# Kernel tuning notes

Measured on AMD Instinct MI355X. Metric: run time of the kernel, lower is better.

## Reference

```python
import jax, jax.numpy as jnp
import numpy as np

NPOINT = 2048
NSAMPLE = 32
BN_EPS = 1e-5


def fps(xyz_t, npoint):
    """Furthest point sampling. xyz_t: [B,N,3] -> idx [B,npoint] (starts at index 0)."""
    B, N, _ = xyz_t.shape

    def step(carry, _):
        dist, last = carry  # dist [B,N], last [B]
        centroid = jnp.take_along_axis(xyz_t, last[:, None, None], axis=1)  # [B,1,3]
        d = jnp.sum((xyz_t - centroid) ** 2, axis=-1)  # [B,N]
        dist = jnp.minimum(dist, d)
        nxt = jnp.argmax(dist, axis=1).astype(jnp.int32)
        return (dist, nxt), last

    init = (jnp.full((B, N), 1e10, xyz_t.dtype), jnp.zeros((B,), jnp.int32))
    _, idx = jax.lax.scan(step, init, None, length=npoint)  # [npoint,B]
    return jnp.transpose(idx)  # [B,npoint]


def knn(k, query_t, ref_t):
    """query_t [B,S,3], ref_t [B,N,3] -> k-nearest indices [B,S,k]."""
    d = (jnp.sum(query_t ** 2, -1)[:, :, None]
         + jnp.sum(ref_t ** 2, -1)[:, None, :]
         - 2.0 * jnp.einsum('bsc,bnc->bsn', query_t, ref_t))  # [B,S,N]
    _, idx = jax.lax.top_k(-d, k)
    return idx


def group(feat_t, idx):
    """feat_t [B,N,C], idx [B,S,K] -> [B,S,K,C] gathered neighbors."""
    return jax.vmap(lambda f, i: f[i])(feat_t, idx)


def setup_inputs():
    key = jax.random.key(0)
    ks = jax.random.split(key, 8)
    B, N, C, D = 8, 8192, 3, 3
    mlp = [32, 32, 64]
    inp = {
        'xyz': jax.random.normal(ks[0], (B, C, N), jnp.float32),
        'points': jax.random.normal(ks[1], (B, D, N), jnp.float32),
    }
    last = D + 3  # conv input channels = in_channel + 3
    for i, oc in enumerate(mlp):
        inp[f'w{i}'] = jax.random.normal(ks[2 + i], (oc, last), jnp.float32) * (1.0 / np.sqrt(last))
        inp[f'g{i}'] = jnp.ones((oc,), jnp.float32)
        inp[f'b{i}'] = jnp.zeros((oc,), jnp.float32)
        last = oc
    return inp


def reference(xyz, points, w0, g0, b0, w1, g1, b1, w2, g2, b2):
    xyz_t = jnp.transpose(xyz, (0, 2, 1))        # [B,N,3]
    points_t = jnp.transpose(points, (0, 2, 1))  # [B,N,D]

    fps_idx = fps(xyz_t, NPOINT)                             # [B,S]
    new_xyz_t = jax.vmap(lambda f, i: f[i])(xyz_t, fps_idx)  # [B,S,3]

    knn_idx = knn(NSAMPLE, new_xyz_t, xyz_t)                 # [B,S,K]
    grouped_xyz = group(xyz_t, knn_idx)                      # [B,S,K,3]
    pos_diff = grouped_xyz - new_xyz_t[:, :, None, :]        # [B,S,K,3]
    grouped_pts = group(points_t, knn_idx)                   # [B,S,K,D]

    x = jnp.concatenate([pos_diff, grouped_pts], axis=-1)    # [B,S,K,3+D]
    for w, g, b in ((w0, g0, b0), (w1, g1, b1), (w2, g2, b2)):
        x = jnp.einsum('oc,bskc->bsko', w, x)                # 1x1 conv, no bias
        mean = jnp.mean(x, axis=(0, 1, 2))                   # BatchNorm2d (training stats)
        var = jnp.var(x, axis=(0, 1, 2))
        x = jax.nn.relu(g * (x - mean) * jax.lax.rsqrt(var + BN_EPS) + b)

    new_points = jnp.max(x, axis=2)  # max over K neighbors -> [B,S,C']
    new_xyz = jnp.transpose(new_xyz_t, (0, 2, 1))      # [B,3,S]
    new_points = jnp.transpose(new_points, (0, 2, 1))  # [B,C',S]
    return (new_xyz, new_points, fps_idx)
```

## Files before the change

kernel.cpp:

```cpp
#include <hip/hip_runtime.h>
#include <hip/hip_bf16.h>
#include <math.h>


#define NB 8
#define NN 8192
#define NS 2048
#define NK 32

__global__ __launch_bounds__(256) void prep_kernel(const float* __restrict__ xyz,
                                                   const float* __restrict__ pts,
                                                   float4* __restrict__ xyz4,
                                                   float4* __restrict__ pts4) {
  int g = blockIdx.x * 256 + threadIdx.x;
  int b = g >> 13, n = g & 8191;
  const float* xb = xyz + b * 3 * NN;
  float x = xb[n], y = xb[NN + n], z = xb[2 * NN + n];
  xyz4[g] = make_float4(x, y, z, fmaf(x, x, fmaf(y, y, z * z)));
  const float* pb = pts + b * 3 * NN;
  pts4[g] = make_float4(pb[n], pb[NN + n], pb[2 * NN + n], 0.f);
}

template <int CTRL>
__device__ __forceinline__ float dpp_max(float v) {
  int o = __builtin_amdgcn_update_dpp(__float_as_int(v), __float_as_int(v),
                                      CTRL, 0xf, 0xf, false);
  return fmaxf(v, __int_as_float(o));
}

__global__ __launch_bounds__(512, 2) void fps_kernel(const float4* __restrict__ xyz4,
                                                     float* __restrict__ out_nxyz,
                                                     float* __restrict__ out_fps,
                                                     float4* __restrict__ nxyz4) {
  __shared__ unsigned long long wslot[2][8];
  int b = blockIdx.x, tid = threadIdx.x;
  int lane = tid & 63, wid = tid >> 6;
  const float4* xb = xyz4 + b * NN;

  float ax[16], ay[16], az[16];
  float dist[16];
#pragma unroll
  for (int j = 0; j < 16; ++j) {
    float4 t = xb[(tid << 4) + j];
    asm volatile("v_accvgpr_write_b32 %0, %1" : "=a"(ax[j]) : "v"(t.x));
    asm volatile("v_accvgpr_write_b32 %0, %1" : "=a"(ay[j]) : "v"(t.y));
    asm volatile("v_accvgpr_write_b32 %0, %1" : "=a"(az[j]) : "v"(t.z));
    dist[j] = 1e10f;
  }

  float4 c0 = xb[0];
  float cx = c0.x, cy = c0.y, cz = c0.z;
  if (tid == 0) {
    nxyz4[b * NS] = c0;
    out_nxyz[b * 3 * NS] = c0.x;
    out_nxyz[b * 3 * NS + NS] = c0.y;
    out_nxyz[b * 3 * NS + 2 * NS] = c0.z;
    out_fps[b * NS] = 0.f;
  }
  __syncthreads();

  for (int s = 1; s < NS; ++s) {
    float best = -1.0f;
    int bj = 0;
#pragma unroll
    for (int j = 0; j < 16; ++j) {
      float x, y, z;
      asm volatile("v_accvgpr_read_b32 %0, %1" : "=v"(x) : "a"(ax[j]));
      asm volatile("v_accvgpr_read_b32 %0, %1" : "=v"(y) : "a"(ay[j]));
      asm volatile("v_accvgpr_read_b32 %0, %1" : "=v"(z) : "a"(az[j]));
      float dx = __fsub_rn(x, cx);
      float dy = __fsub_rn(y, cy);
      float dz = __fsub_rn(z, cz);
      float d = __fadd_rn(__fadd_rn(__fmul_rn(dx, dx), __fmul_rn(dy, dy)),
                          __fmul_rn(dz, dz));
      d = fminf(dist[j], d);
      dist[j] = d;
      bool gt = d > best;
      best = gt ? d : best;
      bj = gt ? j : bj;
    }

    float m = best;
    m = dpp_max<0x111>(m);
    m = dpp_max<0x112>(m);
    m = dpp_max<0x114>(m);
    m = dpp_max<0x118>(m);
    m = dpp_max<0x142>(m);
    m = dpp_max<0x143>(m);
    float wmax = __int_as_float(__builtin_amdgcn_readlane(__float_as_int(m), 63));

    unsigned long long bl = __ballot(best == wmax);
    int l0 = __ffsll(bl) - 1;
    int gcand = (tid << 4) + bj;
    int gw = __builtin_amdgcn_readlane(gcand, l0);

    if (lane == 0)
      wslot[s & 1][wid] = (((unsigned long long)__float_as_uint(wmax)) << 32) |
                          (unsigned)(8191 - gw);
    __syncthreads();

    unsigned long long vm = wslot[s & 1][0];
#pragma unroll
    for (int k = 1; k < 8; ++k) {
      unsigned long long o = wslot[s & 1][k];
      vm = o > vm ? o : vm;
    }
    int gid = 8191 - (int)(unsigned)(vm & 0xFFFFFFFFull);
    gid = __builtin_amdgcn_readfirstlane(gid);

    float4 c = xb[gid];
    cx = c.x; cy = c.y; cz = c.z;
    if (tid == 0) {
      nxyz4[b * NS + s] = c;
      out_nxyz[b * 3 * NS + s] = c.x;
      out_nxyz[b * 3 * NS + NS + s] = c.y;
      out_nxyz[b * 3 * NS + 2 * NS + s] = c.z;
      out_fps[b * NS + s] = (float)gid;
    }
  }
}

__device__ __forceinline__ void insert32(float (&a)[32], float f) {
#pragma unroll
  for (int i = 31; i >= 1; --i) a[i] = fminf(a[i], fmaxf(a[i - 1], f));
  a[0] = fminf(a[0], f);
}

__global__ __launch_bounds__(256) void knn_kernel(const float4* __restrict__ xyz4,
                                                  const float4* __restrict__ nxyz4,
                                                  int* __restrict__ knn) {
  __shared__ float lbuf[256][33];
  int b = blockIdx.x >> 5, tile = blockIdx.x & 31;
  int tid = threadIdx.x;
  int q = tid & 63, chunk = tid >> 6;
  float4 Q = nxyz4[b * NS + tile * 64 + q];
  float qq = Q.w;
  float mx = -2.f * Q.x, my = -2.f * Q.y, mz = -2.f * Q.z;
  float arr[32];
#pragma unroll
  for (int i = 0; i < 32; ++i) arr[i] = __uint_as_float(0x7f7fffffu);

  const float4* refs = xyz4 + b * NN + chunk * 2048;
  int rbase = chunk * 2048;
  for (int r = 0; r < 2048; r += 4) {
    float4 R0 = refs[r];
    float4 R1 = refs[r + 1];
    float4 R2 = refs[r + 2];
    float4 R3 = refs[r + 3];
    float d0 = fmaxf(fmaf(R0.x, mx, fmaf(R0.y, my, fmaf(R0.z, mz, R0.w + qq))), 0.f);
    float d1 = fmaxf(fmaf(R1.x, mx, fmaf(R1.y, my, fmaf(R1.z, mz, R1.w + qq))), 0.f);
    float d2 = fmaxf(fmaf(R2.x, mx, fmaf(R2.y, my, fmaf(R2.z, mz, R2.w + qq))), 0.f);
    float d3 = fmaxf(fmaf(R3.x, mx, fmaf(R3.y, my, fmaf(R3.z, mz, R3.w + qq))), 0.f);
    float f0 = __uint_as_float((__float_as_uint(d0) & 0xFFFFE000u) | (unsigned)(rbase + r));
    float f1 = __uint_as_float((__float_as_uint(d1) & 0xFFFFE000u) | (unsigned)(rbase + r + 1));
    float f2 = __uint_as_float((__float_as_uint(d2) & 0xFFFFE000u) | (unsigned)(rbase + r + 2));
    float f3 = __uint_as_float((__float_as_uint(d3) & 0xFFFFE000u) | (unsigned)(rbase + r + 3));
    if (f0 < arr[31]) insert32(arr, f0);
    if (f1 < arr[31]) insert32(arr, f1);
    if (f2 < arr[31]) insert32(arr, f2);
    if (f3 < arr[31]) insert32(arr, f3);
  }
#pragma unroll
  for (int i = 0; i < 32; ++i) lbuf[tid][i] = arr[i];
  __syncthreads();
  if (tid < 64) {
    for (int c = 1; c < 4; ++c)
      for (int i = 0; i < 32; ++i) {
        float f = lbuf[c * 64 + tid][i];
        if (f < arr[31]) insert32(arr, f);
      }
    int base = (b * NS + tile * 64 + tid) * NK;
#pragma unroll
    for (int i = 0; i < 32; ++i) knn[base + i] = (int)(__float_as_uint(arr[i]) & 0x1FFFu);
  }
}

template <int STAGE>
__global__ __launch_bounds__(256) void mlp_kernel(
    const float4* __restrict__ xyz4, const float4* __restrict__ pts4,
    const float4* __restrict__ nxyz4, const int* __restrict__ knn,
    const float* __restrict__ w0, const float* __restrict__ w1,
    const float* __restrict__ w2, const float* __restrict__ ab,
    float* __restrict__ partials, float* __restrict__ out_np) {
  constexpr int C = (STAGE == 2) ? 64 : 32;
  constexpr int SM = (STAGE == 3) ? 8 * 64 * 32 : 512;
  __shared__ float smem[SM];
  int blk = blockIdx.x;
  int b = blk >> 6, s0 = (blk & 63) * 32;
  int tid = threadIdx.x, sl = tid & 31, ksec = tid >> 5;
  int lane = tid & 63, wid = tid >> 6;
  int s = s0 + sl;
  float4 Q = nxyz4[b * NS + s];
  const float4* xb = xyz4 + b * NN;
  const float4* pb = pts4 + b * NN;
  const int* kb = knn + (b * NS + s) * NK + ksec * 4;

  float acc1[(STAGE == 3) ? 64 : C];
  float acc2[(STAGE == 3) ? 1 : C];
  if constexpr (STAGE == 3) {
#pragma unroll
    for (int o = 0; o < 64; ++o) acc1[o] = -3.4e38f;
  } else {
#pragma unroll
    for (int o = 0; o < C; ++o) { acc1[o] = 0.f; acc2[o] = 0.f; }
  }

  for (int kk = 0; kk < 4; ++kk) {
    int nid = kb[kk];
    float4 R = xb[nid];
    float4 P = pb[nid];
    float x0[6] = {R.x - Q.x, R.y - Q.y, R.z - Q.z, P.x, P.y, P.z};
    float h[32];
#pragma unroll
    for (int o = 0; o < 32; ++o) {
      float a = w0[o * 6] * x0[0];
#pragma unroll
      for (int c = 1; c < 6; ++c) a = fmaf(w0[o * 6 + c], x0[c], a);
      h[o] = a;
    }
    if constexpr (STAGE == 0) {
#pragma unroll
      for (int o = 0; o < 32; ++o) { acc1[o] += h[o]; acc2[o] = fmaf(h[o], h[o], acc2[o]); }
    } else {
#pragma unroll
      for (int o = 0; o < 32; ++o) h[o] = fmaxf(fmaf(h[o], ab[o], ab[64 + o]), 0.f);
      float h1[32];
#pragma unroll
      for (int o = 0; o < 32; ++o) {
        float a = 0.f;
#pragma unroll
        for (int i = 0; i < 32; ++i) a = fmaf(w1[o * 32 + i], h[i], a);
        h1[o] = a;
      }
      if constexpr (STAGE == 1) {
#pragma unroll
        for (int o = 0; o < 32; ++o) { acc1[o] += h1[o]; acc2[o] = fmaf(h1[o], h1[o], acc2[o]); }
      } else {
#pragma unroll
        for (int o = 0; o < 32; ++o) h1[o] = fmaxf(fmaf(h1[o], ab[128 + o], ab[192 + o]), 0.f);
#pragma unroll
        for (int o = 0; o < 64; ++o) {
          float a = 0.f;
#pragma unroll
          for (int i = 0; i < 32; ++i) a = fmaf(w2[o * 32 + i], h1[i], a);
          if constexpr (STAGE == 2) {
            acc1[o] += a;
            acc2[o] = fmaf(a, a, acc2[o]);
          } else {
            acc1[o] = fmaxf(acc1[o], fmaxf(fmaf(a, ab[256 + o], ab[320 + o]), 0.f));
          }
        }
      }
    }
  }

  if constexpr (STAGE < 3) {
#pragma unroll
    for (int o = 0; o < C; ++o) {
      float v1 = acc1[o], v2 = acc2[o];
#pragma unroll
      for (int d = 1; d < 64; d <<= 1) { v1 += __shfl_xor(v1, d); v2 += __shfl_xor(v2, d); }
      acc1[o] = v1; acc2[o] = v2;
    }
    if (lane == 0) {
#pragma unroll
      for (int o = 0; o < C; ++o) {
        smem[wid * 2 * C + o] = acc1[o];
        smem[wid * 2 * C + C + o] = acc2[o];
      }
    }
    __syncthreads();
    if (tid < 2 * C) {
      float v = smem[tid] + smem[2 * C + tid] + smem[4 * C + tid] + smem[6 * C + tid];
      partials[blk * 128 + tid] = v;
    }
  } else {
#pragma unroll
    for (int o = 0; o < 64; ++o) smem[ksec * 2048 + o * 32 + sl] = acc1[o];
    __syncthreads();
#pragma unroll
    for (int i = 0; i < 8; ++i) {
      int e = i * 256 + tid;
      int ch = e >> 5, ss = e & 31;
      float v = smem[ch * 32 + ss];
#pragma unroll
      for (int ks = 1; ks < 8; ++ks) v = fmaxf(v, smem[ks * 2048 + ch * 32 + ss]);
      out_np[b * 64 * NS + ch * NS + s0 + ss] = v;
    }
  }
}

__global__ __launch_bounds__(256) void finalize_kernel(const float* __restrict__ partials,
                                                       const float* __restrict__ g,
                                                       const float* __restrict__ bt,
                                                       float* __restrict__ ab, int C) {
  __shared__ float sm[256];
  int tid = threadIdx.x;
  int ch = tid & 127, half = tid >> 7;
  float acc = 0.f;
  if (ch < 2 * C) {
    const float* p = partials + half * 256 * 128 + ch;
    for (int i = 0; i < 256; ++i) acc += p[i * 128];
  }
  sm[half * 128 + ch] = acc;
  __syncthreads();
  if (tid < C) {
    float s1 = sm[tid] + sm[128 + tid];
    float s2 = sm[C + tid] + sm[128 + C + tid];
    const float ninv = 1.0f / 524288.0f;
    float mean = s1 * ninv;
    float var = s2 * ninv - mean * mean;
    float inv = 1.0f / sqrtf(var + 1e-5f);
    float a = g[tid] * inv;
    ab[tid] = a;
    ab[64 + tid] = bt[tid] - mean * a;
  }
}

extern "C" void kernel_launch(void* const* d_in, const int* in_sizes, int n_in,
                              void* d_out, int out_size, void* d_ws, size_t ws_size,
                              hipStream_t stream) {
  const float* xyz = (const float*)d_in[0];
  const float* pts = (const float*)d_in[1];
  const float* w0 = (const float*)d_in[2];
  const float* g0 = (const float*)d_in[3];
  const float* b0 = (const float*)d_in[4];
  const float* w1 = (const float*)d_in[5];
  const float* g1 = (const float*)d_in[6];
  const float* b1 = (const float*)d_in[7];
  const float* w2 = (const float*)d_in[8];
  const float* g2 = (const float*)d_in[9];
  const float* b2 = (const float*)d_in[10];
  float* out = (float*)d_out;
  float* ws = (float*)d_ws;

  float4* xyz4 = (float4*)ws;
  float4* pts4 = (float4*)(ws + 262144);
  float4* nxyz4 = (float4*)(ws + 524288);
  int* knn = (int*)(ws + 589824);
  float* partials = ws + 1114112;
  float* ab = ws + 1310720;
  float* out_np = out + 49152;
  float* out_fps = out + 1097728;

  prep_kernel<<<256, 256, 0, stream>>>(xyz, pts, xyz4, pts4);
  fps_kernel<<<NB, 512, 0, stream>>>(xyz4, out, out_fps, nxyz4);
  knn_kernel<<<256, 256, 0, stream>>>(xyz4, nxyz4, knn);

  mlp_kernel<0><<<512, 256, 0, stream>>>(xyz4, pts4, nxyz4, knn, w0, w1, w2, ab, partials, nullptr);
  finalize_kernel<<<1, 256, 0, stream>>>(partials, g0, b0, ab, 32);
  mlp_kernel<1><<<512, 256, 0, stream>>>(xyz4, pts4, nxyz4, knn, w0, w1, w2, ab, partials + 65536, nullptr);
  finalize_kernel<<<1, 256, 0, stream>>>(partials + 65536, g1, b1, ab + 128, 32);
  mlp_kernel<2><<<512, 256, 0, stream>>>(xyz4, pts4, nxyz4, knn, w0, w1, w2, ab, partials + 131072, nullptr);
  finalize_kernel<<<1, 256, 0, stream>>>(partials + 131072, g2, b2, ab + 256, 64);
  mlp_kernel<3><<<512, 256, 0, stream>>>(xyz4, pts4, nxyz4, knn, w0, w1, w2, ab, nullptr, out_np);
}
```

Baseline: 3.265 ms.

## Fuse FPS, KNN and first BN stats into one persistent kernel with progress flags

Merges the FPS, KNN and stage-0 MLP statistics into a single mega-kernel. Eight blocks run FPS and publish progress every 64 samples through a release flag, while the KNN blocks spin-wait on that flag and start as soon as their tile of centroids exists. This overlaps KNN with the serial FPS loop and removes the separate mlp stage-0 pass. The per-block partial buffers are replaced by global atomicAdd accumulation, which shrinks the finalize kernel, and the FPS argmax is restructured to a max pass plus a search on the winning lane only. The spin-wait needs every FPS block to be resident alongside the waiting blocks; if the 8 FPS blocks are not scheduled, the kernel deadlocks.

```diff
diff --git a/kernel.cpp b/kernel.cpp
--- a/kernel.cpp
+++ b/kernel.cpp
@@ -11,8 +11,15 @@
 __global__ __launch_bounds__(256) void prep_kernel(const float* __restrict__ xyz,
                                                    const float* __restrict__ pts,
                                                    float4* __restrict__ xyz4,
-                                                   float4* __restrict__ pts4) {
-  int g = blockIdx.x * 256 + threadIdx.x;
+                                                   float4* __restrict__ pts4,
+                                                   float* __restrict__ stats_acc,
+                                                   int* __restrict__ prog) {
+  int tid = threadIdx.x;
+  if (blockIdx.x == 0) {
+    stats_acc[tid] = 0.f;
+    if (tid < 8) prog[tid] = 0;
+  }
+  int g = blockIdx.x * 256 + tid;
   int b = g >> 13, n = g & 8191;
   const float* xb = xyz + b * 3 * NN;
   float x = xb[n], y = xb[NN + n], z = xb[2 * NN + n];
@@ -28,140 +35,158 @@
   return fmaxf(v, __int_as_float(o));
 }
 
-__global__ __launch_bounds__(512, 2) void fps_kernel(const float4* __restrict__ xyz4,
-                                                     float* __restrict__ out_nxyz,
-                                                     float* __restrict__ out_fps,
-                                                     float4* __restrict__ nxyz4) {
-  __shared__ unsigned long long wslot[2][8];
-  int b = blockIdx.x, tid = threadIdx.x;
-  int lane = tid & 63, wid = tid >> 6;
-  const float4* xb = xyz4 + b * NN;
-
-  float ax[16], ay[16], az[16];
-  float dist[16];
-#pragma unroll
-  for (int j = 0; j < 16; ++j) {
-    float4 t = xb[(tid << 4) + j];
-    asm volatile("v_accvgpr_write_b32 %0, %1" : "=a"(ax[j]) : "v"(t.x));
-    asm volatile("v_accvgpr_write_b32 %0, %1" : "=a"(ay[j]) : "v"(t.y));
-    asm volatile("v_accvgpr_write_b32 %0, %1" : "=a"(az[j]) : "v"(t.z));
-    dist[j] = 1e10f;
-  }
-
-  float4 c0 = xb[0];
-  float cx = c0.x, cy = c0.y, cz = c0.z;
-  if (tid == 0) {
-    nxyz4[b * NS] = c0;
-    out_nxyz[b * 3 * NS] = c0.x;
-    out_nxyz[b * 3 * NS + NS] = c0.y;
-    out_nxyz[b * 3 * NS + 2 * NS] = c0.z;
-    out_fps[b * NS] = 0.f;
-  }
-  __syncthreads();
-
-  for (int s = 1; s < NS; ++s) {
-    float best = -1.0f;
-    int bj = 0;
-#pragma unroll
-    for (int j = 0; j < 16; ++j) {
-      float x, y, z;
-      asm volatile("v_accvgpr_read_b32 %0, %1" : "=v"(x) : "a"(ax[j]));
-      asm volatile("v_accvgpr_read_b32 %0, %1" : "=v"(y) : "a"(ay[j]));
-      asm volatile("v_accvgpr_read_b32 %0, %1" : "=v"(z) : "a"(az[j]));
-      float dx = __fsub_rn(x, cx);
-      float dy = __fsub_rn(y, cy);
-      float dz = __fsub_rn(z, cz);
-      float d = __fadd_rn(__fadd_rn(__fmul_rn(dx, dx), __fmul_rn(dy, dy)),
-                          __fmul_rn(dz, dz));
-      d = fminf(dist[j], d);
-      dist[j] = d;
-      bool gt = d > best;
-      best = gt ? d : best;
-      bj = gt ? j : bj;
-    }
-
-    float m = best;
-    m = dpp_max<0x111>(m);
-    m = dpp_max<0x112>(m);
-    m = dpp_max<0x114>(m);
-    m = dpp_max<0x118>(m);
-    m = dpp_max<0x142>(m);
-    m = dpp_max<0x143>(m);
-    float wmax = __int_as_float(__builtin_amdgcn_readlane(__float_as_int(m), 63));
-
-    unsigned long long bl = __ballot(best == wmax);
-    int l0 = __ffsll(bl) - 1;
-    int gcand = (tid << 4) + bj;
-    int gw = __builtin_amdgcn_readlane(gcand, l0);
-
-    if (lane == 0)
-      wslot[s & 1][wid] = (((unsigned long long)__float_as_uint(wmax)) << 32) |
-                          (unsigned)(8191 - gw);
-    __syncthreads();
-
-    unsigned long long vm = wslot[s & 1][0];
-#pragma unroll
-    for (int k = 1; k < 8; ++k) {
-      unsigned long long o = wslot[s & 1][k];
-      vm = o > vm ? o : vm;
-    }
-    int gid = 8191 - (int)(unsigned)(vm & 0xFFFFFFFFull);
-    gid = __builtin_amdgcn_readfirstlane(gid);
-
-    float4 c = xb[gid];
-    cx = c.x; cy = c.y; cz = c.z;
-    if (tid == 0) {
-      nxyz4[b * NS + s] = c;
-      out_nxyz[b * 3 * NS + s] = c.x;
-      out_nxyz[b * 3 * NS + NS + s] = c.y;
-      out_nxyz[b * 3 * NS + 2 * NS + s] = c.z;
-      out_fps[b * NS + s] = (float)gid;
-    }
-  }
-}
-
 __device__ __forceinline__ void insert32(float (&a)[32], float f) {
 #pragma unroll
   for (int i = 31; i >= 1; --i) a[i] = fminf(a[i], fmaxf(a[i - 1], f));
   a[0] = fminf(a[0], f);
 }
 
-__global__ __launch_bounds__(256) void knn_kernel(const float4* __restrict__ xyz4,
-                                                  const float4* __restrict__ nxyz4,
-                                                  int* __restrict__ knn) {
+__global__ __launch_bounds__(512, 1) void mega_kernel(
+    const float4* __restrict__ xyz4, const float4* __restrict__ pts4,
+    float4* __restrict__ nxyz4, int* __restrict__ knn,
+    const float* __restrict__ w0, float* __restrict__ stats_acc,
+    int* __restrict__ prog, float* __restrict__ out_nxyz,
+    float* __restrict__ out_fps) {
   __shared__ float lbuf[256][33];
-  int b = blockIdx.x >> 5, tile = blockIdx.x & 31;
+  __shared__ unsigned long long wslot[2][8];
   int tid = threadIdx.x;
-  int q = tid & 63, chunk = tid >> 6;
-  float4 Q = nxyz4[b * NS + tile * 64 + q];
-  float qq = Q.w;
-  float mx = -2.f * Q.x, my = -2.f * Q.y, mz = -2.f * Q.z;
+  int lane = tid & 63, wid = tid >> 6;
+
+  if (blockIdx.x < 8) {
+    int b = blockIdx.x;
+    const float4* xb = xyz4 + b * NN;
+
+    float ax[16], ay[16], az[16], dist[16];
+#pragma unroll
+    for (int j = 0; j < 16; ++j) {
+      float4 t = xb[(tid << 4) + j];
+      asm volatile("v_accvgpr_write_b32 %0, %1" : "=a"(ax[j]) : "v"(t.x));
+      asm volatile("v_accvgpr_write_b32 %0, %1" : "=a"(ay[j]) : "v"(t.y));
+      asm volatile("v_accvgpr_write_b32 %0, %1" : "=a"(az[j]) : "v"(t.z));
+      dist[j] = 1e10f;
+    }
+    float4 c0 = xb[0];
+    float cx = c0.x, cy = c0.y, cz = c0.z;
+    if (tid == 0) {
+      nxyz4[b * NS] = c0;
+      out_nxyz[b * 3 * NS] = c0.x;
+      out_nxyz[b * 3 * NS + NS] = c0.y;
+      out_nxyz[b * 3 * NS + 2 * NS] = c0.z;
+      out_fps[b * NS] = 0.f;
+    }
+    __syncthreads();
+
+    for (int s = 1; s < NS; ++s) {
+#pragma unroll
+      for (int j = 0; j < 16; ++j) {
+        float x, y, z;
+        asm volatile("v_accvgpr_read_b32 %0, %1" : "=v"(x) : "a"(ax[j]));
+        asm volatile("v_accvgpr_read_b32 %0, %1" : "=v"(y) : "a"(ay[j]));
+        asm volatile("v_accvgpr_read_b32 %0, %1" : "=v"(z) : "a"(az[j]));
+        float dx = __fsub_rn(x, cx);
+        float dy = __fsub_rn(y, cy);
+        float dz = __fsub_rn(z, cz);
+        float d = __fadd_rn(__fadd_rn(__fmul_rn(dx, dx), __fmul_rn(dy, dy)),
+                            __fmul_rn(dz, dz));
+        dist[j] = fminf(dist[j], d);
+      }
+      float lmax = dist[0];
+#pragma unroll
+      for (int j = 1; j < 16; ++j) lmax = fmaxf(lmax, dist[j]);
+
+      float m = lmax;
+      m = dpp_max<0x111>(m);
+      m = dpp_max<0x112>(m);
+      m = dpp_max<0x114>(m);
+      m = dpp_max<0x118>(m);
+      m = dpp_max<0x142>(m);
+      m = dpp_max<0x143>(m);
+      float wmax = __int_as_float(__builtin_amdgcn_readlane(__float_as_int(m), 63));
+
+      unsigned long long bl = __ballot(lmax == wmax);
+      int l0 = __ffsll(bl) - 1;
+      int bj = 0;
+      if (lmax == wmax) {
+#pragma unroll
+        for (int t = 15; t >= 0; --t)
+          if (dist[t] == lmax) bj = t;
+      }
+      int gcand = (tid << 4) + bj;
+      int gw = __builtin_amdgcn_readlane(gcand, l0);
+
+      if (lane == 0)
+        wslot[s & 1][wid] = (((unsigned long long)__float_as_uint(wmax)) << 32) |
+                            (unsigned)(8191 - gw);
+      __syncthreads();
+
+      unsigned long long vm = wslot[s & 1][0];
+#pragma unroll
+      for (int k = 1; k < 8; ++k) {
+        unsigned long long o = wslot[s & 1][k];
+        vm = o > vm ? o : vm;
+      }
+      int gid = 8191 - (int)(unsigned)(vm & 0xFFFFFFFFull);
+      gid = __builtin_amdgcn_readfirstlane(gid);
+
+      float4 c = xb[gid];
+      cx = c.x; cy = c.y; cz = c.z;
+      if (tid == 0) {
+        nxyz4[b * NS + s] = c;
+        out_nxyz[b * 3 * NS + s] = c.x;
+        out_nxyz[b * 3 * NS + NS + s] = c.y;
+        out_nxyz[b * 3 * NS + 2 * NS + s] = c.z;
+        out_fps[b * NS + s] = (float)gid;
+        if (((s + 1) & 63) == 0) {
+          __threadfence();
+          __hip_atomic_store(&prog[b], s + 1, __ATOMIC_RELEASE,
+                             __HIP_MEMORY_SCOPE_AGENT);
+        }
+      }
+    }
+    return;
+  }
+
+  int idx = blockIdx.x - 8;
+  int b = idx >> 5, tile = idx & 31;
+  const float4* xb = xyz4 + b * NN;
+  const float4* pb = pts4 + b * NN;
+
+  if (tid == 0) {
+    int need = (tile + 1) * 64;
+    while (__hip_atomic_load(&prog[b], __ATOMIC_ACQUIRE,
+                             __HIP_MEMORY_SCOPE_AGENT) < need)
+      __builtin_amdgcn_s_sleep(64);
+  }
+  __syncthreads();
+
   float arr[32];
-#pragma unroll
-  for (int i = 0; i < 32; ++i) arr[i] = __uint_as_float(0x7f7fffffu);
-
-  const float4* refs = xyz4 + b * NN + chunk * 2048;
-  int rbase = chunk * 2048;
-  for (int r = 0; r < 2048; r += 4) {
-    float4 R0 = refs[r];
-    float4 R1 = refs[r + 1];
-    float4 R2 = refs[r + 2];
-    float4 R3 = refs[r + 3];
-    float d0 = fmaxf(fmaf(R0.x, mx, fmaf(R0.y, my, fmaf(R0.z, mz, R0.w + qq))), 0.f);
-    float d1 = fmaxf(fmaf(R1.x, mx, fmaf(R1.y, my, fmaf(R1.z, mz, R1.w + qq))), 0.f);
-    float d2 = fmaxf(fmaf(R2.x, mx, fmaf(R2.y, my, fmaf(R2.z, mz, R2.w + qq))), 0.f);
-    float d3 = fmaxf(fmaf(R3.x, mx, fmaf(R3.y, my, fmaf(R3.z, mz, R3.w + qq))), 0.f);
-    float f0 = __uint_as_float((__float_as_uint(d0) & 0xFFFFE000u) | (unsigned)(rbase + r));
-    float f1 = __uint_as_float((__float_as_uint(d1) & 0xFFFFE000u) | (unsigned)(rbase + r + 1));
-    float f2 = __uint_as_float((__float_as_uint(d2) & 0xFFFFE000u) | (unsigned)(rbase + r + 2));
-    float f3 = __uint_as_float((__float_as_uint(d3) & 0xFFFFE000u) | (unsigned)(rbase + r + 3));
-    if (f0 < arr[31]) insert32(arr, f0);
-    if (f1 < arr[31]) insert32(arr, f1);
-    if (f2 < arr[31]) insert32(arr, f2);
-    if (f3 < arr[31]) insert32(arr, f3);
-  }
-#pragma unroll
-  for (int i = 0; i < 32; ++i) lbuf[tid][i] = arr[i];
+  if (tid < 256) {
+    int q = tid & 63, chunk = tid >> 6;
+    float4 Q = nxyz4[b * NS + tile * 64 + q];
+    float qq = Q.w;
+    float mx = -2.f * Q.x, my = -2.f * Q.y, mz = -2.f * Q.z;
+#pragma unroll
+    for (int i = 0; i < 32; ++i) arr[i] = __uint_as_float(0x7f7fffffu);
+    const float4* refs = xb + chunk * 2048;
+    int rbase = chunk * 2048;
+    for (int r = 0; r < 2048; r += 4) {
+      float4 R0 = refs[r], R1 = refs[r + 1], R2 = refs[r + 2], R3 = refs[r + 3];
+      float d0 = fmaxf(fmaf(R0.x, mx, fmaf(R0.y, my, fmaf(R0.z, mz, R0.w + qq))), 0.f);
+      float d1 = fmaxf(fmaf(R1.x, mx, fmaf(R1.y, my, fmaf(R1.z, mz, R1.w + qq))), 0.f);
+      float d2 = fmaxf(fmaf(R2.x, mx, fmaf(R2.y, my, fmaf(R2.z, mz, R2.w + qq))), 0.f);
+      float d3 = fmaxf(fmaf(R3.x, mx, fmaf(R3.y, my, fmaf(R3.z, mz, R3.w + qq))), 0.f);
+      float f0 = __uint_as_float((__float_as_uint(d0) & 0xFFFFE000u) | (unsigned)(rbase + r));
+      float f1 = __uint_as_float((__float_as_uint(d1) & 0xFFFFE000u) | (unsigned)(rbase + r + 1));
+      float f2 = __uint_as_float((__float_as_uint(d2) & 0xFFFFE000u) | (unsigned)(rbase + r + 2));
+      float f3 = __uint_as_float((__float_as_uint(d3) & 0xFFFFE000u) | (unsigned)(rbase + r + 3));
+      if (f0 < arr[31]) insert32(arr, f0);
+      if (f1 < arr[31]) insert32(arr, f1);
+      if (f2 < arr[31]) insert32(arr, f2);
+      if (f3 < arr[31]) insert32(arr, f3);
+    }
+#pragma unroll
+    for (int i = 0; i < 32; ++i) lbuf[tid][i] = arr[i];
+  }
   __syncthreads();
   if (tid < 64) {
     for (int c = 1; c < 4; ++c)
@@ -171,7 +196,55 @@
       }
     int base = (b * NS + tile * 64 + tid) * NK;
 #pragma unroll
-    for (int i = 0; i < 32; ++i) knn[base + i] = (int)(__float_as_uint(arr[i]) & 0x1FFFu);
+    for (int i = 0; i < 32; ++i) {
+      knn[base + i] = (int)(__float_as_uint(arr[i]) & 0x1FFFu);
+      lbuf[tid][i] = arr[i];
+    }
+  }
+  __syncthreads();
+
+  float sum[32], sumsq[32];
+#pragma unroll
+  for (int o = 0; o < 32; ++o) { sum[o] = 0.f; sumsq[o] = 0.f; }
+  for (int t = 0; t < 4; ++t) {
+    int e = tid * 4 + t;
+    int sq = e >> 5, k = e & 31;
+    int nid = (int)(__float_as_uint(lbuf[sq][k]) & 0x1FFFu);
+    float4 Q = nxyz4[b * NS + tile * 64 + sq];
+    float4 R = xb[nid];
+    float4 P = pb[nid];
+    float x0[6] = {R.x - Q.x, R.y - Q.y, R.z - Q.z, P.x, P.y, P.z};
+#pragma unroll
+    for (int o = 0; o < 32; ++o) {
+      float a = w0[o * 6] * x0[0];
+#pragma unroll
+      for (int c = 1; c < 6; ++c) a = fmaf(w0[o * 6 + c], x0[c], a);
+      sum[o] += a;
+      sumsq[o] = fmaf(a, a, sumsq[o]);
+    }
+  }
+#pragma unroll
+  for (int o = 0; o < 32; ++o) {
+    float s = sum[o], q = sumsq[o];
+#pragma unroll
+    for (int d = 1; d < 64; d <<= 1) { s += __shfl_xor(s, d); q += __shfl_xor(q, d); }
+    sum[o] = s; sumsq[o] = q;
+  }
+  __syncthreads();
+  float* cmb = &lbuf[0][0];
+  if (lane == 0) {
+#pragma unroll
+    for (int o = 0; o < 32; ++o) {
+      cmb[wid * 64 + o] = sum[o];
+      cmb[wid * 64 + 32 + o] = sumsq[o];
+    }
+  }
+  __syncthreads();
+  if (tid < 64) {
+    float tot = 0.f;
+#pragma unroll
+    for (int w = 0; w < 8; ++w) tot += cmb[w * 64 + tid];
+    atomicAdd(&stats_acc[tid], tot);
   }
 }
 
@@ -181,7 +254,7 @@
     const float4* __restrict__ nxyz4, const int* __restrict__ knn,
     const float* __restrict__ w0, const float* __restrict__ w1,
     const float* __restrict__ w2, const float* __restrict__ ab,
-    float* __restrict__ partials, float* __restrict__ out_np) {
+    float* __restrict__ acc, float* __restrict__ out_np) {
   constexpr int C = (STAGE == 2) ? 64 : 32;
   constexpr int SM = (STAGE == 3) ? 8 * 64 * 32 : 512;
   __shared__ float smem[SM];
@@ -216,39 +289,32 @@
       float a = w0[o * 6] * x0[0];
 #pragma unroll
       for (int c = 1; c < 6; ++c) a = fmaf(w0[o * 6 + c], x0[c], a);
-      h[o] = a;
-    }
-    if constexpr (STAGE == 0) {
-#pragma unroll
-      for (int o = 0; o < 32; ++o) { acc1[o] += h[o]; acc2[o] = fmaf(h[o], h[o], acc2[o]); }
+      h[o] = fmaxf(fmaf(a, ab[o], ab[64 + o]), 0.f);
+    }
+    float h1[32];
+#pragma unroll
+    for (int o = 0; o < 32; ++o) {
+      float a = 0.f;
+#pragma unroll
+      for (int i = 0; i < 32; ++i) a = fmaf(w1[o * 32 + i], h[i], a);
+      h1[o] = a;
+    }
+    if constexpr (STAGE == 1) {
+#pragma unroll
+      for (int o = 0; o < 32; ++o) { acc1[o] += h1[o]; acc2[o] = fmaf(h1[o], h1[o], acc2[o]); }
     } else {
 #pragma unroll
-      for (int o = 0; o < 32; ++o) h[o] = fmaxf(fmaf(h[o], ab[o], ab[64 + o]), 0.f);
-      float h1[32];
-#pragma unroll
-      for (int o = 0; o < 32; ++o) {
+      for (int o = 0; o < 32; ++o) h1[o] = fmaxf(fmaf(h1[o], ab[128 + o], ab[192 + o]), 0.f);
+#pragma unroll
+      for (int o = 0; o < 64; ++o) {
         float a = 0.f;
 #pragma unroll
-        for (int i = 0; i < 32; ++i) a = fmaf(w1[o * 32 + i], h[i], a);
-        h1[o] = a;
-      }
-      if constexpr (STAGE == 1) {
-#pragma unroll
-        for (int o = 0; o < 32; ++o) { acc1[o] += h1[o]; acc2[o] = fmaf(h1[o], h1[o], acc2[o]); }
-      } else {
-#pragma unroll
-        for (int o = 0; o < 32; ++o) h1[o] = fmaxf(fmaf(h1[o], ab[128 + o], ab[192 + o]), 0.f);
-#pragma unroll
-        for (int o = 0; o < 64; ++o) {
-          float a = 0.f;
-#pragma unroll
-          for (int i = 0; i < 32; ++i) a = fmaf(w2[o * 32 + i], h1[i], a);
-          if constexpr (STAGE == 2) {
-            acc1[o] += a;
-            acc2[o] = fmaf(a, a, acc2[o]);
-          } else {
-            acc1[o] = fmaxf(acc1[o], fmaxf(fmaf(a, ab[256 + o], ab[320 + o]), 0.f));
-          }
+        for (int i = 0; i < 32; ++i) a = fmaf(w2[o * 32 + i], h1[i], a);
+        if constexpr (STAGE == 2) {
+          acc1[o] += a;
+          acc2[o] = fmaf(a, a, acc2[o]);
+        } else {
+          acc1[o] = fmaxf(acc1[o], fmaxf(fmaf(a, ab[256 + o], ab[320 + o]), 0.f));
         }
       }
     }
@@ -272,7 +338,7 @@
     __syncthreads();
     if (tid < 2 * C) {
       float v = smem[tid] + smem[2 * C + tid] + smem[4 * C + tid] + smem[6 * C + tid];
-      partials[blk * 128 + tid] = v;
+      atomicAdd(&acc[tid], v);
     }
   } else {
 #pragma unroll
@@ -290,23 +356,14 @@
   }
 }
 
-__global__ __launch_bounds__(256) void finalize_kernel(const float* __restrict__ partials,
-                                                       const float* __restrict__ g,
-                                                       const float* __restrict__ bt,
-                                                       float* __restrict__ ab, int C) {
-  __shared__ float sm[256];
+__global__ __launch_bounds__(64) void finalize_kernel(const float* __restrict__ acc,
+                                                      const float* __restrict__ g,
+                                                      const float* __restrict__ bt,
+                                                      float* __restrict__ ab, int C) {
   int tid = threadIdx.x;
-  int ch = tid & 127, half = tid >> 7;
-  float acc = 0.f;
-  if (ch < 2 * C) {
-    const float* p = partials + half * 256 * 128 + ch;
-    for (int i = 0; i < 256; ++i) acc += p[i * 128];
-  }
-  sm[half * 128 + ch] = acc;
-  __syncthreads();
   if (tid < C) {
-    float s1 = sm[tid] + sm[128 + tid];
-    float s2 = sm[C + tid] + sm[128 + C + tid];
+    float s1 = acc[tid];
+    float s2 = acc[C + tid];
     const float ninv = 1.0f / 524288.0f;
     float mean = s1 * ninv;
     float var = s2 * ninv - mean * mean;
@@ -338,20 +395,22 @@
   float4* pts4 = (float4*)(ws + 262144);
   float4* nxyz4 = (float4*)(ws + 524288);
   int* knn = (int*)(ws + 589824);
-  float* partials = ws + 1114112;
-  float* ab = ws + 1310720;
+  float* stats_acc = ws + 1114112;
+  int* prog = (int*)(ws + 1114368);
+  float* ab = ws + 1114432;
   float* out_np = out + 49152;
   float* out_fps = out + 1097728;
 
-  prep_kernel<<<256, 256, 0, stream>>>(xyz, pts, xyz4, pts4);
-  fps_kernel<<<NB, 512, 0, stream>>>(xyz4, out, out_fps, nxyz4);
-  knn_kernel<<<256, 256, 0, stream>>>(xyz4, nxyz4, knn);
-
-  mlp_kernel<0><<<512, 256, 0, stream>>>(xyz4, pts4, nxyz4, knn, w0, w1, w2, ab, partials, nullptr);
-  finalize_kernel<<<1, 256, 0, stream>>>(partials, g0, b0, ab, 32);
-  mlp_kernel<1><<<512, 256, 0, stream>>>(xyz4, pts4, nxyz4, knn, w0, w1, w2, ab, partials + 65536, nullptr);
-  finalize_kernel<<<1, 256, 0, stream>>>(partials + 65536, g1, b1, ab + 128, 32);
-  mlp_kernel<2><<<512, 256, 0, stream>>>(xyz4, pts4, nxyz4, knn, w0, w1, w2, ab, partials + 131072, nullptr);
-  finalize_kernel<<<1, 256, 0, stream>>>(partials + 131072, g2, b2, ab + 256, 64);
-  mlp_kernel<3><<<512, 256, 0, stream>>>(xyz4, pts4, nxyz4, knn, w0, w1, w2, ab, nullptr, out_np);
-}
+  prep_kernel<<<256, 256, 0, stream>>>(xyz, pts, xyz4, pts4, stats_acc, prog);
+  mega_kernel<<<264, 512, 0, stream>>>(xyz4, pts4, nxyz4, knn, w0, stats_acc,
+                                       prog, out, out_fps);
+  finalize_kernel<<<1, 64, 0, stream>>>(stats_acc, g0, b0, ab, 32);
+  mlp_kernel<1><<<512, 256, 0, stream>>>(xyz4, pts4, nxyz4, knn, w0, w1, w2, ab,
+                                         stats_acc + 64, nullptr);
+  finalize_kernel<<<1, 64, 0, stream>>>(stats_acc + 64, g1, b1, ab + 128, 32);
+  mlp_kernel<2><<<512, 256, 0, stream>>>(xyz4, pts4, nxyz4, knn, w0, w1, w2, ab,
+                                         stats_acc + 128, nullptr);
+  finalize_kernel<<<1, 64, 0, stream>>>(stats_acc + 128, g2, b2, ab + 256, 64);
+  mlp_kernel<3><<<512, 256, 0, stream>>>(xyz4, pts4, nxyz4, knn, w0, w1, w2, ab,
+                                         nullptr, out_np);
+}
```

Result: slower. 3.900 ms (+19.4%).
